# Kernel tuning notes

Hardware: AMD Instinct MI355X
Metric: run time of the kernel (lower is better)

Reference implementation:

```python
import jax, jax.numpy as jnp
import numpy as np

LOSS1_COEFF = 1.0
LOSS2_COEFF = 1.0
LOSS3_COEFF = 1.0
LOSS4_COEFF = 0.5


def smooth_l1(x, y):
    # torch smooth_l1_loss, beta=1, reduction='mean'
    d = jnp.abs(x - y)
    return jnp.mean(jnp.where(d < 1.0, 0.5 * d * d, d - 0.5))


def setup_inputs() -> dict:
    key = jax.random.key(0)
    k1, k2 = jax.random.split(key)
    B, N, F = 256, 8192, 13
    targets = jax.random.uniform(k1, (B, N, F), dtype=jnp.float32)
    preds = jax.random.uniform(k2, (B, N, F), dtype=jnp.float32)
    return {"targets": targets, "preds": preds}


def reference(targets, preds):
    tb = targets[:, :, :4]  # [B,N,4]
    pb = preds[:, :, :4]
    # The original builds a [B,N,N] pairwise IoU matrix and takes its diagonal;
    # the diagonal is exactly the elementwise matched-pair IoU, computed here directly.
    xx1 = jnp.maximum(tb[..., 0], pb[..., 0])
    yy1 = jnp.maximum(tb[..., 1], pb[..., 1])
    xx2 = jnp.minimum(tb[..., 2], pb[..., 2])
    yy2 = jnp.minimum(tb[..., 3], pb[..., 3])
    w = jnp.clip(xx2 - xx1, 0.0)
    h = jnp.clip(yy2 - yy1, 0.0)
    inter = w * h
    area1 = (tb[..., 2] - tb[..., 0]) * (tb[..., 3] - tb[..., 1])
    area2 = (pb[..., 2] - pb[..., 0]) * (pb[..., 3] - pb[..., 1])
    ious = inter / (area1 + area2 - inter + 1e-07)  # [B,N]

    loss1 = smooth_l1(jnp.ones_like(ious), ious)
    loss2 = smooth_l1(tb, pb)
    loss3 = smooth_l1(targets[:, :, -1], preds[:, :, -1])
    loss4 = smooth_l1(targets[:, :, 4:12], preds[:, :, 4:12])
    return (LOSS1_COEFF * loss1 + LOSS2_COEFF * loss2
            + LOSS3_COEFF * loss3 + LOSS4_COEFF * loss4)
```

## Files before the change

kernel.cpp:

```cpp
#include <hip/hip_runtime.h>
#include <hip/hip_bf16.h>


#define ROWS_TOTAL   (256 * 8192)
#define ROWS_PER_BLK 256
#define FLOATS_PER_CHUNK (ROWS_PER_BLK * 13)
#define F4_PER_CHUNK (FLOATS_PER_CHUNK / 4)

__device__ __forceinline__ float sl1(float d) {
    d = fabsf(d);
    return d < 1.0f ? 0.5f * d * d : d - 0.5f;
}

__global__ __launch_bounds__(256) void loss_kernel(const float* __restrict__ targets,
                                                   const float* __restrict__ preds,
                                                   float* __restrict__ out) {
    __shared__ float st[FLOATS_PER_CHUNK];
    __shared__ float sp[FLOATS_PER_CHUNK];
    __shared__ float wave_part[4];

    const int tid   = threadIdx.x;
    const int chunk = blockIdx.x;
    const long long base = (long long)chunk * FLOATS_PER_CHUNK;

    const float4* gt = (const float4*)(targets + base);
    const float4* gp = (const float4*)(preds + base);
    float4* lt = (float4*)st;
    float4* lp = (float4*)sp;
#pragma unroll
    for (int k = 0; k < 4; ++k) {
        int i = k * 256 + tid;
        if (i < F4_PER_CHUNK) {
            lt[i] = gt[i];
            lp[i] = gp[i];
        }
    }
    __syncthreads();

    const int rb = tid * 13;
    float t0 = st[rb+0],  t1 = st[rb+1],  t2 = st[rb+2],  t3 = st[rb+3];
    float p0 = sp[rb+0],  p1 = sp[rb+1],  p2 = sp[rb+2],  p3 = sp[rb+3];

    float s2 = sl1(t0-p0) + sl1(t1-p1) + sl1(t2-p2) + sl1(t3-p3);

    float s4 = 0.0f;
#pragma unroll
    for (int f = 4; f < 12; ++f) s4 += sl1(st[rb+f] - sp[rb+f]);

    float s3 = sl1(st[rb+12] - sp[rb+12]);

    float xx1 = fmaxf(t0, p0);
    float yy1 = fmaxf(t1, p1);
    float xx2 = fminf(t2, p2);
    float yy2 = fminf(t3, p3);
    float w = fmaxf(xx2 - xx1, 0.0f);
    float h = fmaxf(yy2 - yy1, 0.0f);
    float inter = w * h;
    float area1 = (t2 - t0) * (t3 - t1);
    float area2 = (p2 - p0) * (p3 - p1);
    float iou = inter / (area1 + area2 - inter + 1e-7f);
    float s1 = sl1(1.0f - iou);

    constexpr float W1 = 1.0f / 2097152.0f;
    constexpr float W2 = 1.0f / 8388608.0f;
    constexpr float W3 = 1.0f / 2097152.0f;
    constexpr float W4 = 1.0f / 33554432.0f;

    float c = W1 * s1 + W2 * s2 + W3 * s3 + W4 * s4;

#pragma unroll
    for (int off = 32; off > 0; off >>= 1)
        c += __shfl_down(c, off, 64);

    const int wave = tid >> 6;
    const int lane = tid & 63;
    if (lane == 0) wave_part[wave] = c;
    __syncthreads();
    if (tid == 0) {
        float blk = wave_part[0] + wave_part[1] + wave_part[2] + wave_part[3];
        atomicAdd(out, blk);
    }
}

extern "C" void kernel_launch(void* const* d_in, const int* in_sizes, int n_in,
                              void* d_out, int out_size, void* d_ws, size_t ws_size,
                              hipStream_t stream) {
    const float* targets = (const float*)d_in[0];
    const float* preds   = (const float*)d_in[1];
    float* out = (float*)d_out;

    hipMemsetAsync(out, 0, sizeof(float), stream);

    const int blocks = ROWS_TOTAL / ROWS_PER_BLK;
    loss_kernel<<<blocks, 256, 0, stream>>>(targets, preds, out);
}
```

Before: 276.5 us.

## Use persistent blocks with register prefetch and two-stage reduction

Replaces the one-chunk-per-block grid with 1536 persistent blocks that loop over chunks, prefetching the next chunk into registers while computing the current one from shared memory. The global atomicAdd and the memset are replaced by per-block partials written to workspace and summed by a second single-block kernel. The aim is to overlap loads with compute and cut launch, scheduling and atomic overhead. In exchange it adds a second kernel launch and an extra barrier on every iteration.

```diff
diff --git a/kernel.cpp b/kernel.cpp
--- a/kernel.cpp
+++ b/kernel.cpp
@@ -2,84 +2,117 @@
 #include <hip/hip_bf16.h>
 
 
-#define ROWS_TOTAL   (256 * 8192)
-#define ROWS_PER_BLK 256
-#define FLOATS_PER_CHUNK (ROWS_PER_BLK * 13)
-#define F4_PER_CHUNK (FLOATS_PER_CHUNK / 4)
+#define NCHUNK          8192
+#define ROWS_PER_CHUNK  256
+#define FPC             (ROWS_PER_CHUNK * 13)
+#define F4PC            (FPC / 4)
+#define NBLK            1536
 
 __device__ __forceinline__ float sl1(float d) {
     d = fabsf(d);
     return d < 1.0f ? 0.5f * d * d : d - 0.5f;
 }
 
-__global__ __launch_bounds__(256) void loss_kernel(const float* __restrict__ targets,
-                                                   const float* __restrict__ preds,
-                                                   float* __restrict__ out) {
-    __shared__ float st[FLOATS_PER_CHUNK];
-    __shared__ float sp[FLOATS_PER_CHUNK];
-    __shared__ float wave_part[4];
+__global__ __launch_bounds__(256) void loss_stage1(const float* __restrict__ T,
+                                                   const float* __restrict__ P,
+                                                   float* __restrict__ partial) {
+    __shared__ float st[FPC];
+    __shared__ float sp[FPC];
+    __shared__ float wred[4];
 
-    const int tid   = threadIdx.x;
-    const int chunk = blockIdx.x;
-    const long long base = (long long)chunk * FLOATS_PER_CHUNK;
+    const int tid = threadIdx.x;
+    float4 at[4], ap[4];
 
-    const float4* gt = (const float4*)(targets + base);
-    const float4* gp = (const float4*)(preds + base);
-    float4* lt = (float4*)st;
-    float4* lp = (float4*)sp;
+    int c = blockIdx.x;
+
+    {
+        const float4* gt = (const float4*)(T + (long long)c * FPC);
+        const float4* gp = (const float4*)(P + (long long)c * FPC);
 #pragma unroll
-    for (int k = 0; k < 4; ++k) {
-        int i = k * 256 + tid;
-        if (i < F4_PER_CHUNK) {
-            lt[i] = gt[i];
-            lp[i] = gp[i];
+        for (int k = 0; k < 4; ++k) {
+            int i = k * 256 + tid;
+            if (i < F4PC) { at[k] = gt[i]; ap[k] = gp[i]; }
         }
     }
-    __syncthreads();
 
-    const int rb = tid * 13;
-    float t0 = st[rb+0],  t1 = st[rb+1],  t2 = st[rb+2],  t3 = st[rb+3];
-    float p0 = sp[rb+0],  p1 = sp[rb+1],  p2 = sp[rb+2],  p3 = sp[rb+3];
+    float acc = 0.0f;
+    while (c < NCHUNK) {
+        const int cn = c + NBLK;
 
-    float s2 = sl1(t0-p0) + sl1(t1-p1) + sl1(t2-p2) + sl1(t3-p3);
+        float4* lt = (float4*)st;
+        float4* lp = (float4*)sp;
+#pragma unroll
+        for (int k = 0; k < 4; ++k) {
+            int i = k * 256 + tid;
+            if (i < F4PC) { lt[i] = at[k]; lp[i] = ap[k]; }
+        }
+        __syncthreads();
 
-    float s4 = 0.0f;
+        if (cn < NCHUNK) {
+            const float4* gt = (const float4*)(T + (long long)cn * FPC);
+            const float4* gp = (const float4*)(P + (long long)cn * FPC);
 #pragma unroll
-    for (int f = 4; f < 12; ++f) s4 += sl1(st[rb+f] - sp[rb+f]);
+            for (int k = 0; k < 4; ++k) {
+                int i = k * 256 + tid;
+                if (i < F4PC) { at[k] = gt[i]; ap[k] = gp[i]; }
+            }
+        }
 
-    float s3 = sl1(st[rb+12] - sp[rb+12]);
+        const int rb = tid * 13;
+        float t0 = st[rb+0], t1 = st[rb+1], t2 = st[rb+2], t3 = st[rb+3];
+        float p0 = sp[rb+0], p1 = sp[rb+1], p2 = sp[rb+2], p3 = sp[rb+3];
 
-    float xx1 = fmaxf(t0, p0);
-    float yy1 = fmaxf(t1, p1);
-    float xx2 = fminf(t2, p2);
-    float yy2 = fminf(t3, p3);
-    float w = fmaxf(xx2 - xx1, 0.0f);
-    float h = fmaxf(yy2 - yy1, 0.0f);
-    float inter = w * h;
-    float area1 = (t2 - t0) * (t3 - t1);
-    float area2 = (p2 - p0) * (p3 - p1);
-    float iou = inter / (area1 + area2 - inter + 1e-7f);
-    float s1 = sl1(1.0f - iou);
+        float s2 = sl1(t0-p0) + sl1(t1-p1) + sl1(t2-p2) + sl1(t3-p3);
 
-    constexpr float W1 = 1.0f / 2097152.0f;
-    constexpr float W2 = 1.0f / 8388608.0f;
-    constexpr float W3 = 1.0f / 2097152.0f;
-    constexpr float W4 = 1.0f / 33554432.0f;
+        float s4 = 0.0f;
+#pragma unroll
+        for (int f = 4; f < 12; ++f) s4 += sl1(st[rb+f] - sp[rb+f]);
 
-    float c = W1 * s1 + W2 * s2 + W3 * s3 + W4 * s4;
+        float s3 = sl1(st[rb+12] - sp[rb+12]);
+
+        float xx1 = fmaxf(t0, p0);
+        float yy1 = fmaxf(t1, p1);
+        float xx2 = fminf(t2, p2);
+        float yy2 = fminf(t3, p3);
+        float w = fmaxf(xx2 - xx1, 0.0f);
+        float h = fmaxf(yy2 - yy1, 0.0f);
+        float inter = w * h;
+        float a1 = (t2 - t0) * (t3 - t1);
+        float a2 = (p2 - p0) * (p3 - p1);
+        float iou = inter / (a1 + a2 - inter + 1e-7f);
+        float s1 = sl1(1.0f - iou);
+
+        constexpr float W1 = 1.0f / 2097152.0f;
+        constexpr float W2 = 1.0f / 8388608.0f;
+        constexpr float W3 = 1.0f / 2097152.0f;
+        constexpr float W4 = 1.0f / 33554432.0f;
+        acc += W1*s1 + W2*s2 + W3*s3 + W4*s4;
+
+        __syncthreads();
+        c = cn;
+    }
 
 #pragma unroll
     for (int off = 32; off > 0; off >>= 1)
-        c += __shfl_down(c, off, 64);
+        acc += __shfl_down(acc, off, 64);
+    if ((tid & 63) == 0) wred[tid >> 6] = acc;
+    __syncthreads();
+    if (tid == 0)
+        partial[blockIdx.x] = wred[0] + wred[1] + wred[2] + wred[3];
+}
 
-    const int wave = tid >> 6;
-    const int lane = tid & 63;
-    if (lane == 0) wave_part[wave] = c;
+__global__ __launch_bounds__(256) void loss_stage2(const float* __restrict__ partial,
+                                                   float* __restrict__ out) {
+    __shared__ float wred[4];
+    const int tid = threadIdx.x;
+    float a = 0.0f;
+    for (int i = tid; i < NBLK; i += 256) a += partial[i];
+#pragma unroll
+    for (int off = 32; off > 0; off >>= 1)
+        a += __shfl_down(a, off, 64);
+    if ((tid & 63) == 0) wred[tid >> 6] = a;
     __syncthreads();
-    if (tid == 0) {
-        float blk = wave_part[0] + wave_part[1] + wave_part[2] + wave_part[3];
-        atomicAdd(out, blk);
-    }
+    if (tid == 0) out[0] = wred[0] + wred[1] + wred[2] + wred[3];
 }
 
 extern "C" void kernel_launch(void* const* d_in, const int* in_sizes, int n_in,
@@ -87,10 +120,9 @@
                               hipStream_t stream) {
     const float* targets = (const float*)d_in[0];
     const float* preds   = (const float*)d_in[1];
-    float* out = (float*)d_out;
+    float* out     = (float*)d_out;
+    float* partial = (float*)d_ws;
 
-    hipMemsetAsync(out, 0, sizeof(float), stream);
-
-    const int blocks = ROWS_TOTAL / ROWS_PER_BLK;
-    loss_kernel<<<blocks, 256, 0, stream>>>(targets, preds, out);
+    loss_stage1<<<NBLK, 256, 0, stream>>>(targets, preds, partial);
+    loss_stage2<<<1, 256, 0, stream>>>(partial, out);
 }
```

Result: faster. 269.0 us (-2.7%).
